# Kernel optimization log

Hardware: AMD Instinct MI355X
Metric: run time of the kernel (lower is better)

## Reference

```python
import jax, jax.numpy as jnp
import numpy as np

EPS = 0.05
N_ITER = 50
IN_DIM = 4096
PROJ_DIM = 128
BATCH = 4096


def sinkhorn_loss(x, y, eps=EPS, n_iter=N_ITER):
    # x, y: [B, N, D]
    B, N, _ = x.shape
    # squared euclidean cost, matches torch.cdist(p=2).pow(2): [B, N, N]
    C = jnp.sum((x[:, :, None, :] - y[:, None, :, :]) ** 2, axis=-1)
    log_K = -C / eps
    log_ab = -jnp.log(jnp.asarray(N, x.dtype))  # log_a = log_b = -log N
    log_u0 = jnp.zeros((B, N), x.dtype)
    log_v0 = jnp.zeros((B, N), x.dtype)

    def step(carry, _):
        log_u, log_v = carry
        log_u = log_ab - jax.scipy.special.logsumexp(log_K + log_v[:, None, :], axis=-1)
        log_v = log_ab - jax.scipy.special.logsumexp(log_K + log_u[:, :, None], axis=-2)
        return (log_u, log_v), None

    (log_u, log_v), _ = jax.lax.scan(step, (log_u0, log_v0), None, length=n_iter)
    log_T = log_K + log_u[:, :, None] + log_v[:, None, :]
    T = jnp.exp(log_T)
    transport_cost = jnp.sum(T * C, axis=(1, 2))
    entropic = eps * jnp.sum(T * (log_T - 1.0), axis=(1, 2))
    return jnp.mean(transport_cost + entropic)


def setup_inputs() -> dict:
    key = jax.random.key(0)
    ks = jax.random.split(key, 6)
    scale = 1.0 / np.sqrt(IN_DIM)
    return {
        "x_ct": jax.random.normal(ks[0], (BATCH, IN_DIM), jnp.float32),
        "x_txt": jax.random.normal(ks[1], (BATCH, IN_DIM), jnp.float32),
        "x_lab": jax.random.normal(ks[2], (BATCH, IN_DIM), jnp.float32),
        "W_ct": jax.random.uniform(ks[3], (PROJ_DIM, IN_DIM), jnp.float32, -scale, scale),
        "W_txt": jax.random.uniform(ks[4], (PROJ_DIM, IN_DIM), jnp.float32, -scale, scale),
        "W_lab": jax.random.uniform(ks[5], (PROJ_DIM, IN_DIM), jnp.float32, -scale, scale),
    }


def reference(x_ct, x_txt, x_lab, W_ct, W_txt, W_lab):
    # Linear projections (no bias): z = x @ W.T -> [B, P]
    z_ct = x_ct @ W_ct.T
    z_txt = x_txt @ W_txt.T
    z_lab = x_lab @ W_lab.T
    # unsqueeze(1): each becomes a point cloud of N=1 points
    z_ct_e = z_ct[:, None, :]
    z_txt_e = z_txt[:, None, :]
    z_lab_e = z_lab[:, None, :]
    loss_ct_txt = sinkhorn_loss(z_ct_e, z_txt_e)
    loss_ct_lab = sinkhorn_loss(z_ct_e, z_lab_e)
    loss_txt_lab = sinkhorn_loss(z_txt_e, z_lab_e)
    ot_loss = (loss_ct_txt + loss_ct_lab + loss_txt_lab) / 3.0
    aligned = (z_ct + z_txt + z_lab) / 3.0
    return (aligned, ot_loss)
```

## Files before the change

### kernel.cpp

```cpp
#include <hip/hip_runtime.h>
#include <stdint.h>

typedef __attribute__((ext_vector_type(8))) short short8;
typedef __attribute__((ext_vector_type(4))) float f32x4;
typedef __attribute__((ext_vector_type(4))) uint32_t u32x4;

#define K_DIM 4096
#define N_DIM 128
#define M_DIM 4096
#define MN ((size_t)M_DIM * N_DIM)
#define NS 8
#define BK 32
#define FRAG_PER_SLAB ((size_t)64 * 8192)

__device__ __forceinline__ uint16_t f2bf(float f) {
    uint32_t u = __float_as_uint(f);
    return (uint16_t)((u + 0x7FFFu + ((u >> 16) & 1u)) >> 16);
}
__device__ __forceinline__ float bf2f(uint16_t h) {
    return __uint_as_float((uint32_t)h << 16);
}

__device__ __forceinline__ short8 cvt8(const float4 lo, const float4 hi) {
    short8 r;
    r[0] = (short)f2bf(lo.x); r[1] = (short)f2bf(lo.y);
    r[2] = (short)f2bf(lo.z); r[3] = (short)f2bf(lo.w);
    r[4] = (short)f2bf(hi.x); r[5] = (short)f2bf(hi.y);
    r[6] = (short)f2bf(hi.z); r[7] = (short)f2bf(hi.w);
    return r;
}

__global__ __launch_bounds__(256) void prep_kernel(
    const float* __restrict__ W0, const float* __restrict__ W1,
    const float* __restrict__ W2, uint16_t* __restrict__ Wb)
{
    int gid = blockIdx.x * 256 + threadIdx.x;
    int g = gid >> 16;
    int e = (gid & 65535) * 8;
    const float* W = (g == 0) ? W0 : (g == 1) ? W1 : W2;
    float4 lo = *(const float4*)(W + e);
    float4 hi = *(const float4*)(W + e + 4);
    *(short8*)(Wb + (size_t)g * (N_DIM * K_DIM) + e) = cvt8(lo, hi);
}

__global__ __launch_bounds__(256, 6) void gemm3_kernel(
    const float* __restrict__ x0, const float* __restrict__ x1,
    const float* __restrict__ x2, const uint16_t* __restrict__ Wb,
    uint16_t* __restrict__ zpart)
{
    __shared__ uint16_t lds[2][4096];

    const int tid  = threadIdx.x;
    const int lane = tid & 63;
    const int wv   = tid >> 6;

    const int per = (192 * NS) >> 3;
    const int lid = (blockIdx.x & 7) * per + (blockIdx.x >> 3);
    const int g   = lid / (NS * 64);
    const int rem = lid % (NS * 64);
    const int ks  = rem >> 6;
    const int mt  = rem & 63;
    const int k0  = ks * (K_DIM / NS);
    const int NT  = (K_DIM / NS) / BK;

    const float* x = (g == 0) ? x0 : (g == 1) ? x1 : x2;
    const uint16_t* Wg = Wb + (size_t)g * (N_DIM * K_DIM);

    const int c16 = lane & 15;
    const int qg  = lane >> 4;
    const int rowbase = mt * 64 + wv * 16;
    const float* aptr = x + (size_t)(rowbase + c16) * K_DIM + qg * 8 + k0;

    const uint16_t* wsrc[2];
#pragma unroll
    for (int c = 0; c < 2; ++c) {
        const int e    = c * 2048 + tid * 8;
        const int col  = e >> 5;
        const int slot = (e >> 3) & 3;
        wsrc[c] = Wg + (size_t)col * K_DIM + (slot ^ ((col >> 1) & 3)) * 8 + k0;
    }

    f32x4 acc[8];
#pragma unroll
    for (int nf = 0; nf < 8; ++nf) acc[nf] = (f32x4)0.f;

    auto stage = [&](int p, int kbase) {
#pragma unroll
        for (int c = 0; c < 2; ++c) {
            __builtin_amdgcn_global_load_lds(
                (const __attribute__((address_space(1))) uint32_t*)(wsrc[c] + kbase),
                (__attribute__((address_space(3))) uint32_t*)&lds[p][c * 2048 + wv * 512],
                16, 0, 0);
        }
    };

    stage(0, 0);
    float4 a_cur[2], a_nxt[2];
    a_cur[0] = *(const float4*)(aptr);
    a_cur[1] = *(const float4*)(aptr + 4);

    const int cswz = (c16 >> 1) & 3;
    const int sswz = (qg ^ cswz) * 8;

    int p = 0;
    for (int kt = 0; kt < NT; ++kt) {
        const int kbase = kt * BK;
        __syncthreads();
        if (kt + 1 < NT) {
            stage(p ^ 1, kbase + BK);
            const float* ap = aptr + kbase + BK;
            a_nxt[0] = *(const float4*)(ap);
            a_nxt[1] = *(const float4*)(ap + 4);
        }
        short8 af = cvt8(a_cur[0], a_cur[1]);
#pragma unroll
        for (int nf = 0; nf < 8; ++nf) {
            short8 bf = *(const short8*)&lds[p][(nf * 16 + c16) * 32 + sswz];
            acc[nf] = __builtin_amdgcn_mfma_f32_16x16x32_bf16(af, bf, acc[nf], 0, 0, 0);
        }
        a_cur[0] = a_nxt[0];
        a_cur[1] = a_nxt[1];
        p ^= 1;
    }

    uint32_t dw[16];
#pragma unroll
    for (int nf = 0; nf < 8; ++nf) {
        dw[nf * 2]     = (uint32_t)f2bf(acc[nf][0]) | ((uint32_t)f2bf(acc[nf][1]) << 16);
        dw[nf * 2 + 1] = (uint32_t)f2bf(acc[nf][2]) | ((uint32_t)f2bf(acc[nf][3]) << 16);
    }
    uint16_t* zp = zpart + (size_t)(ks * 3 + g) * FRAG_PER_SLAB
                 + (size_t)mt * 8192 + (size_t)(wv * 64 + lane) * 32;
    uint32_t* zp32 = (uint32_t*)zp;
#pragma unroll
    for (int j = 0; j < 4; ++j) {
        u32x4 v = { dw[j * 4], dw[j * 4 + 1], dw[j * 4 + 2], dw[j * 4 + 3] };
        *(u32x4*)(zp32 + j * 4) = v;
    }
}

__global__ __launch_bounds__(256) void combine_kernel(
    const uint16_t* __restrict__ zpart, float* __restrict__ out,
    float* __restrict__ partials)
{
    const int tid  = threadIdx.x;
    const int gtid = blockIdx.x * 256 + tid;
    const size_t F0 = (size_t)gtid * 8;

    const int idx_base = (int)(F0 & 31);
    const int lane = (int)((F0 >> 5) & 63);
    const int wv   = (int)((F0 >> 11) & 3);
    const int mt   = (int)(F0 >> 13);
    const int c16  = lane & 15;
    const int qg   = lane >> 4;
    const int rowb = mt * 64 + wv * 16 + qg * 4;

    float zs[3][8];
#pragma unroll
    for (int g = 0; g < 3; ++g)
#pragma unroll
        for (int v = 0; v < 8; ++v) zs[g][v] = 0.f;

#pragma unroll
    for (int ks = 0; ks < NS; ++ks) {
#pragma unroll
        for (int g = 0; g < 3; ++g) {
            const short8 pv = *(const short8*)(zpart + (size_t)(ks * 3 + g) * FRAG_PER_SLAB + F0);
#pragma unroll
            for (int v = 0; v < 8; ++v) zs[g][v] += bf2f((uint16_t)pv[v]);
        }
    }

    float s = 0.f;
#pragma unroll
    for (int v = 0; v < 8; ++v) {
        const float a = zs[0][v], b = zs[1][v], c = zs[2][v];
        const int idx = idx_base + v;
        const int nf = idx >> 2, r = idx & 3;
        out[(size_t)(rowb + r) * N_DIM + nf * 16 + c16] = (a + b + c) * (1.f / 3.f);
        const float d1 = a - b, d2 = a - c, d3 = b - c;
        s += d1 * d1 + d2 * d2 + d3 * d3;
    }

#pragma unroll
    for (int off = 32; off > 0; off >>= 1) s += __shfl_xor(s, off);
    __shared__ float wsum[4];
    if ((tid & 63) == 0) wsum[tid >> 6] = s;
    __syncthreads();
    if (tid == 0) partials[blockIdx.x] = wsum[0] + wsum[1] + wsum[2] + wsum[3];
}

__global__ __launch_bounds__(256) void finalize_kernel(
    const float* __restrict__ partials, float* __restrict__ out)
{
    const int tid = threadIdx.x;
    float s = partials[tid];
#pragma unroll
    for (int off = 32; off > 0; off >>= 1) s += __shfl_xor(s, off);
    __shared__ float wsum[4];
    if ((tid & 63) == 0) wsum[tid >> 6] = s;
    __syncthreads();
    if (tid == 0)
        out[MN] = (wsum[0] + wsum[1] + wsum[2] + wsum[3]) * (1.f / 12288.f) - 0.05f;
}

extern "C" void kernel_launch(void* const* d_in, const int* in_sizes, int n_in,
                              void* d_out, int out_size, void* d_ws, size_t ws_size,
                              hipStream_t stream)
{
    const float* x0 = (const float*)d_in[0];
    const float* x1 = (const float*)d_in[1];
    const float* x2 = (const float*)d_in[2];
    const float* W0 = (const float*)d_in[3];
    const float* W1 = (const float*)d_in[4];
    const float* W2 = (const float*)d_in[5];
    float* out = (float*)d_out;

    const size_t zpart_bytes = (size_t)NS * 3 * FRAG_PER_SLAB * sizeof(uint16_t);
    const size_t wb_bytes    = (size_t)3 * N_DIM * K_DIM * sizeof(uint16_t);

    char* ws = (char*)d_ws;
    uint16_t* zpart    = (uint16_t*)ws;
    uint16_t* Wb       = (uint16_t*)(ws + zpart_bytes);
    float*    partials = (float*)(ws + zpart_bytes + wb_bytes);

    prep_kernel    <<< 768, 256, 0, stream>>>(W0, W1, W2, Wb);
    gemm3_kernel   <<<1536, 256, 0, stream>>>(x0, x1, x2, Wb, zpart);
    combine_kernel <<< 256, 256, 0, stream>>>(zpart, out, partials);
    finalize_kernel<<<   1, 256, 0, stream>>>(partials, out);
}
```

Before: 59.47 us.

## Halve split-K count and deepen GEMM prefetch to a 4-slot pipeline

Reduces the split-K factor from 8 to 4, so each block covers twice the K range and the grid drops to 768 blocks. The main loop becomes fully unrolled with four LDS/register slots and a prefetch distance of two, using explicit s_waitcnt vmcnt/lgkmcnt and raw s_barrier in place of __syncthreads. Partial-sum traffic through zpart is halved and loads get more time to land before use. In exchange LDS per block doubles and occupancy hint falls from 6 to 3 blocks, and the combine kernel still loops over NS, now 4 slabs.

```diff
diff --git a/kernel.cpp b/kernel.cpp
--- a/kernel.cpp
+++ b/kernel.cpp
@@ -9,9 +9,10 @@
 #define N_DIM 128
 #define M_DIM 4096
 #define MN ((size_t)M_DIM * N_DIM)
-#define NS 8
+#define NS 4
 #define BK 32
-#define FRAG_PER_SLAB ((size_t)64 * 8192)
+#define NTI 32
+#define FRAG_PER_SLAB MN
 
 __device__ __forceinline__ uint16_t f2bf(float f) {
     uint32_t u = __float_as_uint(f);
@@ -43,25 +44,23 @@
     *(short8*)(Wb + (size_t)g * (N_DIM * K_DIM) + e) = cvt8(lo, hi);
 }
 
-__global__ __launch_bounds__(256, 6) void gemm3_kernel(
+__global__ __launch_bounds__(256, 3) void gemm3_kernel(
     const float* __restrict__ x0, const float* __restrict__ x1,
     const float* __restrict__ x2, const uint16_t* __restrict__ Wb,
     uint16_t* __restrict__ zpart)
 {
-    __shared__ uint16_t lds[2][4096];
+    __shared__ uint16_t lds[4][4096];
 
     const int tid  = threadIdx.x;
     const int lane = tid & 63;
     const int wv   = tid >> 6;
 
-    const int per = (192 * NS) >> 3;
-    const int lid = (blockIdx.x & 7) * per + (blockIdx.x >> 3);
-    const int g   = lid / (NS * 64);
-    const int rem = lid % (NS * 64);
+    const int lid = (blockIdx.x & 7) * 96 + (blockIdx.x >> 3);
+    const int g   = lid >> 8;
+    const int rem = lid & 255;
     const int ks  = rem >> 6;
     const int mt  = rem & 63;
     const int k0  = ks * (K_DIM / NS);
-    const int NT  = (K_DIM / NS) / BK;
 
     const float* x = (g == 0) ? x0 : (g == 1) ? x1 : x2;
     const uint16_t* Wg = Wb + (size_t)g * (N_DIM * K_DIM);
@@ -71,57 +70,75 @@
     const int rowbase = mt * 64 + wv * 16;
     const float* aptr = x + (size_t)(rowbase + c16) * K_DIM + qg * 8 + k0;
 
-    const uint16_t* wsrc[2];
-#pragma unroll
-    for (int c = 0; c < 2; ++c) {
-        const int e    = c * 2048 + tid * 8;
-        const int col  = e >> 5;
-        const int slot = (e >> 3) & 3;
-        wsrc[c] = Wg + (size_t)col * K_DIM + (slot ^ ((col >> 1) & 3)) * 8 + k0;
-    }
-
-    f32x4 acc[8];
-#pragma unroll
-    for (int nf = 0; nf < 8; ++nf) acc[nf] = (f32x4)0.f;
-
-    auto stage = [&](int p, int kbase) {
-#pragma unroll
-        for (int c = 0; c < 2; ++c) {
-            __builtin_amdgcn_global_load_lds(
-                (const __attribute__((address_space(1))) uint32_t*)(wsrc[c] + kbase),
-                (__attribute__((address_space(3))) uint32_t*)&lds[p][c * 2048 + wv * 512],
-                16, 0, 0);
-        }
-    };
-
-    stage(0, 0);
-    float4 a_cur[2], a_nxt[2];
-    a_cur[0] = *(const float4*)(aptr);
-    a_cur[1] = *(const float4*)(aptr + 4);
+    const uint16_t* wsrc0;
+    const uint16_t* wsrc1;
+    {
+        const int e0 = tid * 8, e1 = 2048 + tid * 8;
+        const int col0 = e0 >> 5, s0 = (e0 >> 3) & 3;
+        const int col1 = e1 >> 5, s1 = (e1 >> 3) & 3;
+        wsrc0 = Wg + (size_t)col0 * K_DIM + (s0 ^ ((col0 >> 1) & 3)) * 8 + k0;
+        wsrc1 = Wg + (size_t)col1 * K_DIM + (s1 ^ ((col1 >> 1) & 3)) * 8 + k0;
+    }
 
     const int cswz = (c16 >> 1) & 3;
     const int sswz = (qg ^ cswz) * 8;
 
-    int p = 0;
-    for (int kt = 0; kt < NT; ++kt) {
-        const int kbase = kt * BK;
-        __syncthreads();
-        if (kt + 1 < NT) {
-            stage(p ^ 1, kbase + BK);
-            const float* ap = aptr + kbase + BK;
-            a_nxt[0] = *(const float4*)(ap);
-            a_nxt[1] = *(const float4*)(ap + 4);
-        }
-        short8 af = cvt8(a_cur[0], a_cur[1]);
-#pragma unroll
-        for (int nf = 0; nf < 8; ++nf) {
-            short8 bf = *(const short8*)&lds[p][(nf * 16 + c16) * 32 + sswz];
-            acc[nf] = __builtin_amdgcn_mfma_f32_16x16x32_bf16(af, bf, acc[nf], 0, 0, 0);
-        }
-        a_cur[0] = a_nxt[0];
-        a_cur[1] = a_nxt[1];
-        p ^= 1;
-    }
+    f32x4 acc[8];
+#pragma unroll
+    for (int nf = 0; nf < 8; ++nf) acc[nf] = (f32x4)0.f;
+
+    float4 areg[4][2];
+
+#define STAGE(B, KB) do {                                                      \
+    __builtin_amdgcn_global_load_lds(                                          \
+        (const __attribute__((address_space(1))) uint32_t*)(wsrc0 + (KB)),     \
+        (__attribute__((address_space(3))) uint32_t*)&lds[B][wv * 512],        \
+        16, 0, 0);                                                             \
+    __builtin_amdgcn_global_load_lds(                                          \
+        (const __attribute__((address_space(1))) uint32_t*)(wsrc1 + (KB)),     \
+        (__attribute__((address_space(3))) uint32_t*)&lds[B][2048 + wv * 512], \
+        16, 0, 0);                                                             \
+  } while (0)
+
+#define BATCH(B, KB) do {                                                      \
+    STAGE(B, KB);                                                              \
+    areg[B][0] = *(const float4*)(aptr + (KB));                                \
+    areg[B][1] = *(const float4*)(aptr + (KB) + 4);                            \
+  } while (0)
+
+#define ITER(SLOT, KT, VM, ISSUE) do {                                         \
+    asm volatile("s_waitcnt lgkmcnt(0)" ::: "memory");                         \
+    asm volatile("s_barrier" ::: "memory");                                    \
+    if (ISSUE) { BATCH((((SLOT) + 2) & 3), (((KT) + 2) * BK)); }               \
+    asm volatile("s_waitcnt vmcnt(%0)" :: "i"(VM) : "memory");                 \
+    {                                                                          \
+        short8 af = cvt8(areg[SLOT][0], areg[SLOT][1]);                        \
+        _Pragma("unroll")                                                      \
+        for (int nf = 0; nf < 8; ++nf) {                                       \
+            short8 bf = *(const short8*)&lds[SLOT][(nf * 16 + c16) * 32 + sswz]; \
+            acc[nf] = __builtin_amdgcn_mfma_f32_16x16x32_bf16(af, bf, acc[nf], 0, 0, 0); \
+        }                                                                      \
+    }                                                                          \
+  } while (0)
+
+    BATCH(0, 0);
+    BATCH(1, BK);
+
+#pragma unroll
+    for (int kt = 0; kt < 28; kt += 4) {
+        ITER(0, kt + 0, 8, true);
+        ITER(1, kt + 1, 8, true);
+        ITER(2, kt + 2, 8, true);
+        ITER(3, kt + 3, 8, true);
+    }
+    ITER(0, 28, 8, true);
+    ITER(1, 29, 8, true);
+    ITER(2, 30, 4, false);
+    ITER(3, 31, 0, false);
+
+#undef ITER
+#undef BATCH
+#undef STAGE
 
     uint32_t dw[16];
 #pragma unroll
@@ -224,8 +241,8 @@
     uint16_t* Wb       = (uint16_t*)(ws + zpart_bytes);
     float*    partials = (float*)(ws + zpart_bytes + wb_bytes);
 
-    prep_kernel    <<< 768, 256, 0, stream>>>(W0, W1, W2, Wb);
-    gemm3_kernel   <<<1536, 256, 0, stream>>>(x0, x1, x2, Wb, zpart);
-    combine_kernel <<< 256, 256, 0, stream>>>(zpart, out, partials);
-    finalize_kernel<<<   1, 256, 0, stream>>>(partials, out);
-}
+    prep_kernel    <<<768, 256, 0, stream>>>(W0, W1, W2, Wb);
+    gemm3_kernel   <<<768, 256, 0, stream>>>(x0, x1, x2, Wb, zpart);
+    combine_kernel <<<256, 256, 0, stream>>>(zpart, out, partials);
+    finalize_kernel<<<  1, 256, 0, stream>>>(partials, out);
+}
```

After: 55.19 us. 1.08x faster.
